# Kernel tuning notes

Measured on AMD Instinct MI355X. Metric: run time of the kernel, lower is better.

Reference implementation:

```python
import jax, jax.numpy as jnp
import numpy as np

N_HEAD = 8
D = 512
D_K = D // N_HEAD  # 64
B, S = 8, 1024


def setup_inputs() -> dict:
    key = jax.random.key(0)
    ks = jax.random.split(key, 7)
    scale = 1.0 / np.sqrt(D)  # ~ torch Linear init range
    return {
        "q": jax.random.normal(ks[0], (B, S, D), dtype=jnp.float32),
        "k": jax.random.normal(ks[1], (B, S, D), dtype=jnp.float32),
        "v": jax.random.normal(ks[2], (B, S, D), dtype=jnp.float32),
        # per-head Q/K projection weights, torch Linear convention W:[out,in]=[d_k,d]
        "Wq": jax.random.uniform(ks[3], (N_HEAD, D_K, D), jnp.float32, -scale, scale),
        "Wk": jax.random.uniform(ks[4], (N_HEAD, D_K, D), jnp.float32, -scale, scale),
        "Wv": jax.random.uniform(ks[5], (D_K, D), jnp.float32, -scale, scale),
        "Wo": jax.random.uniform(ks[6], (D, D_K), jnpp := jnp.float32, -1.0 / np.sqrt(D_K), 1.0 / np.sqrt(D_K)),
    }


def reference(q, k, v, Wq, Wk, Wv, Wo):
    # shared V projection: [B,S,d_k]
    vs = jnp.einsum("bsd,ed->bse", v, Wv)
    # batched per-head Q/K projections: [B,H,S,d_k]
    qh = jnp.einsum("bsd,hed->bhse", q, Wq)
    kh = jnp.einsum("bsd,hed->bhse", k, Wk)
    inv_sqrt_dk = 1.0 / jnp.sqrt(jnp.asarray(D_K, q.dtype))
    # scores [B,H,Sq,Sk], softmax over keys
    scores = jnp.einsum("bhqe,bhke->bhqk", qh * inv_sqrt_dk, kh)
    attn = jax.nn.softmax(scores, axis=-1)
    # shared V across heads, then mean over heads (interpretable combine)
    heads = jnp.einsum("bhqk,bke->bhqe", attn, vs)  # [B,H,S,d_k]
    head = heads.mean(axis=1)                        # [B,S,d_k]
    out = jnp.einsum("bse,de->bsd", head, Wo)        # [B,S,d]
    # torch.stack(attention) stacks over heads first -> [H,B,Sq,Sk]
    attn_stacked = jnp.transpose(attn, (1, 0, 2, 3))
    return out, attn_stacked
```

## Files before the change

### kernel.cpp

```cpp
#include <hip/hip_runtime.h>


using short8 = __attribute__((ext_vector_type(8))) short;
using f32x4  = __attribute__((ext_vector_type(4))) float;

static __device__ __forceinline__ short f2bf(float f) {
    union { float f; unsigned u; } x; x.f = f;
    unsigned r = x.u + 0x7fffu + ((x.u >> 16) & 1u);
    return (short)(r >> 16);
}
static __device__ __forceinline__ float bfhi2f(unsigned hi_bits) {
    union { unsigned u; float f; } x; x.u = hi_bits;
    return x.f;
}

__global__ __launch_bounds__(256) void proj_all(
    const float* __restrict__ q, const float* __restrict__ k,
    const float* __restrict__ v,
    const float* __restrict__ Wq, const float* __restrict__ Wk,
    const float* __restrict__ Wv,
    short* __restrict__ qh, short* __restrict__ kh, short* __restrict__ vt)
{
    __shared__ short As[128][40];
    __shared__ short Bs[128][40];

    const int y = blockIdx.y;
    const float* A; const float* W; short* out; int N; float scale; int mode; int n0;
    if (y < 4)      { A = q; W = Wq; out = qh; N = 512; scale = 0.125f; mode = 0; n0 = y << 7; }
    else if (y < 8) { A = k; W = Wk; out = kh; N = 512; scale = 1.0f;   mode = 0; n0 = (y - 4) << 7; }
    else            { A = v; W = Wv; out = vt; N = 64;  scale = 1.0f;   mode = 2; n0 = 0; }

    const int K = 512;
    const int tid  = threadIdx.x;
    const int m0   = blockIdx.x * 128;
    const int lane = tid & 63, wave = tid >> 6;
    const int wm   = (wave & 1) * 64, wn = (wave >> 1) * 64;
    const int lrow = lane & 15, lq = lane >> 4;

    f32x4 acc[4][4] = {};

    for (int k0 = 0; k0 < K; k0 += 32) {
#pragma unroll
        for (int i = 0; i < 4; ++i) {
            int c = tid + i * 256;
            int row = c >> 3, c4 = c & 7;
            float4 vv = *(const float4*)(A + (size_t)(m0 + row) * K + k0 + c4 * 4);
            short* dst = &As[row][c4 * 4];
            dst[0] = f2bf(vv.x); dst[1] = f2bf(vv.y); dst[2] = f2bf(vv.z); dst[3] = f2bf(vv.w);
        }
#pragma unroll
        for (int i = 0; i < 4; ++i) {
            int c = tid + i * 256;
            int row = c >> 3, c4 = c & 7;
            int gn = n0 + row;
            float4 vv = make_float4(0.f, 0.f, 0.f, 0.f);
            if (gn < N) vv = *(const float4*)(W + (size_t)gn * K + k0 + c4 * 4);
            short* dst = &Bs[row][c4 * 4];
            dst[0] = f2bf(vv.x); dst[1] = f2bf(vv.y); dst[2] = f2bf(vv.z); dst[3] = f2bf(vv.w);
        }
        __syncthreads();

        short8 af[4], bw[4];
#pragma unroll
        for (int i = 0; i < 4; ++i)
            af[i] = *(const short8*)&As[wm + i * 16 + lrow][lq * 8];
#pragma unroll
        for (int j = 0; j < 4; ++j)
            bw[j] = *(const short8*)&Bs[wn + j * 16 + lrow][lq * 8];
#pragma unroll
        for (int i = 0; i < 4; ++i)
#pragma unroll
            for (int j = 0; j < 4; ++j)
                acc[i][j] = __builtin_amdgcn_mfma_f32_16x16x32_bf16(af[i], bw[j], acc[i][j], 0, 0, 0);
        __syncthreads();
    }

#pragma unroll
    for (int i = 0; i < 4; ++i) {
#pragma unroll
        for (int j = 0; j < 4; ++j) {
#pragma unroll
            for (int r = 0; r < 4; ++r) {
                int m = m0 + wm + i * 16 + lq * 4 + r;
                int n = n0 + wn + j * 16 + lrow;
                if (n >= N) continue;
                float val = acc[i][j][r] * scale;
                if (mode == 0) {
                    int b = m >> 10, s = m & 1023;
                    int hh = n >> 6, e = n & 63;
                    out[(((size_t)(b * 8 + hh) * 1024 + s) << 6) + e] = f2bf(val);
                } else {
                    int b = m >> 10, s = m & 1023;
                    out[(((size_t)b * 64 + n) << 10) + s] = f2bf(val);
                }
            }
        }
    }
}

__global__ __launch_bounds__(256) void gemm_out(
    const float* __restrict__ A, const float* __restrict__ W,
    float* __restrict__ out, int M, int N, int K)
{
    __shared__ short As[128][40];
    __shared__ short Bs[128][40];

    const int tid  = threadIdx.x;
    const int m0   = blockIdx.x * 128;
    const int n0   = blockIdx.y * 128;
    const int lane = tid & 63, wave = tid >> 6;
    const int wm   = (wave & 1) * 64, wn = (wave >> 1) * 64;
    const int lrow = lane & 15, lq = lane >> 4;

    f32x4 acc[4][4] = {};

    for (int k0 = 0; k0 < K; k0 += 32) {
#pragma unroll
        for (int i = 0; i < 4; ++i) {
            int c = tid + i * 256;
            int row = c >> 3, c4 = c & 7;
            float4 vv = *(const float4*)(A + (size_t)(m0 + row) * K + k0 + c4 * 4);
            short* dst = &As[row][c4 * 4];
            dst[0] = f2bf(vv.x); dst[1] = f2bf(vv.y); dst[2] = f2bf(vv.z); dst[3] = f2bf(vv.w);
        }
#pragma unroll
        for (int i = 0; i < 4; ++i) {
            int c = tid + i * 256;
            int row = c >> 3, c4 = c & 7;
            int gn = n0 + row;
            float4 vv = make_float4(0.f, 0.f, 0.f, 0.f);
            if (gn < N) vv = *(const float4*)(W + (size_t)gn * K + k0 + c4 * 4);
            short* dst = &Bs[row][c4 * 4];
            dst[0] = f2bf(vv.x); dst[1] = f2bf(vv.y); dst[2] = f2bf(vv.z); dst[3] = f2bf(vv.w);
        }
        __syncthreads();

        short8 af[4], bw[4];
#pragma unroll
        for (int i = 0; i < 4; ++i)
            af[i] = *(const short8*)&As[wm + i * 16 + lrow][lq * 8];
#pragma unroll
        for (int j = 0; j < 4; ++j)
            bw[j] = *(const short8*)&Bs[wn + j * 16 + lrow][lq * 8];
#pragma unroll
        for (int i = 0; i < 4; ++i)
#pragma unroll
            for (int j = 0; j < 4; ++j)
                acc[i][j] = __builtin_amdgcn_mfma_f32_16x16x32_bf16(af[i], bw[j], acc[i][j], 0, 0, 0);
        __syncthreads();
    }

#pragma unroll
    for (int i = 0; i < 4; ++i)
#pragma unroll
        for (int j = 0; j < 4; ++j)
#pragma unroll
            for (int r = 0; r < 4; ++r) {
                int m = m0 + wm + i * 16 + lq * 4 + r;
                int n = n0 + wn + j * 16 + lrow;
                if (n >= N) continue;
                out[(size_t)m * N + n] = acc[i][j][r];
            }
}

__global__ __launch_bounds__(512) void attn_fused(
    const short* __restrict__ qh,
    const short* __restrict__ kh,
    const short* __restrict__ vt,
    float* __restrict__ attn_out,
    float* __restrict__ head)
{
    __shared__ short qs[128][72];
    __shared__ short ks[128][72];
    __shared__ short vts[64][136];
    __shared__ short pa[8][16][136];

    const int bh = blockIdx.x;
    const int b = bh >> 3, h = bh & 7;
    const int qbase = blockIdx.y << 7;
    const int tid  = threadIdx.x;
    const int lane = tid & 63, wave = tid >> 6;
    const int lrow = lane & 15, lq = lane >> 4;

    const short* qp = qh + ((size_t)bh << 16);
    const short* kp = kh + ((size_t)bh << 16);
    const short* vp = vt + ((size_t)b << 16);

#pragma unroll
    for (int i = 0; i < 2; ++i) {
        int c = tid + i * 512;
        int row = c >> 3, c8 = c & 7;
        *(uint4*)&qs[row][c8 * 8] = *(const uint4*)(qp + (size_t)(qbase + row) * 64 + c8 * 8);
    }
    __syncthreads();

    short8 qf[2];
#pragma unroll
    for (int kk = 0; kk < 2; ++kk)
        qf[kk] = *(const short8*)&qs[wave * 16 + lrow][kk * 32 + lq * 8];

    float sume[4] = {0.f, 0.f, 0.f, 0.f};
    for (int kt = 0; kt < 1024; kt += 128) {
        __syncthreads();
#pragma unroll
        for (int i = 0; i < 2; ++i) {
            int c = tid + i * 512;
            int row = c >> 3, c8 = c & 7;
            *(uint4*)&ks[row][c8 * 8] = *(const uint4*)(kp + (size_t)(kt + row) * 64 + c8 * 8);
        }
        __syncthreads();
#pragma unroll
        for (int j = 0; j < 8; ++j) {
            f32x4 sc = {0.f, 0.f, 0.f, 0.f};
            short8 kb0 = *(const short8*)&ks[j * 16 + lrow][lq * 8];
            short8 kb1 = *(const short8*)&ks[j * 16 + lrow][32 + lq * 8];
            sc = __builtin_amdgcn_mfma_f32_16x16x32_bf16(qf[0], kb0, sc, 0, 0, 0);
            sc = __builtin_amdgcn_mfma_f32_16x16x32_bf16(qf[1], kb1, sc, 0, 0, 0);
#pragma unroll
            for (int r = 0; r < 4; ++r) sume[r] += __expf(sc[r]);
        }
    }
#pragma unroll
    for (int m = 1; m <= 8; m <<= 1)
#pragma unroll
        for (int r = 0; r < 4; ++r) sume[r] += __shfl_xor(sume[r], m, 64);
    float rinv[4];
#pragma unroll
    for (int r = 0; r < 4; ++r) rinv[r] = 1.0f / sume[r];

    f32x4 hacc[4] = {};
    for (int kt = 0; kt < 1024; kt += 128) {
        __syncthreads();
#pragma unroll
        for (int i = 0; i < 2; ++i) {
            int c = tid + i * 512;
            int row = c >> 3, c8 = c & 7;
            *(uint4*)&ks[row][c8 * 8] = *(const uint4*)(kp + (size_t)(kt + row) * 64 + c8 * 8);
        }
#pragma unroll
        for (int i = 0; i < 2; ++i) {
            int c = tid + i * 512;
            int row = c >> 4, c8 = c & 15;
            *(uint4*)&vts[row][c8 * 8] = *(const uint4*)(vp + ((size_t)row << 10) + kt + c8 * 8);
        }
        __syncthreads();

#pragma unroll
        for (int j = 0; j < 8; ++j) {
            f32x4 sc = {0.f, 0.f, 0.f, 0.f};
            short8 kb0 = *(const short8*)&ks[j * 16 + lrow][lq * 8];
            short8 kb1 = *(const short8*)&ks[j * 16 + lrow][32 + lq * 8];
            sc = __builtin_amdgcn_mfma_f32_16x16x32_bf16(qf[0], kb0, sc, 0, 0, 0);
            sc = __builtin_amdgcn_mfma_f32_16x16x32_bf16(qf[1], kb1, sc, 0, 0, 0);
#pragma unroll
            for (int r = 0; r < 4; ++r)
                pa[wave][lq * 4 + r][j * 16 + lrow] = f2bf(__expf(sc[r]) * rinv[r]);
        }

        size_t abase = (((size_t)(h * 8 + b) * 1024 + qbase + wave * 16) << 10) + kt;
#pragma unroll
        for (int i = 0; i < 4; ++i) {
            int c = lane + i * 64;
            int row = c >> 4, c8 = c & 15;
            uint4 pk = *(const uint4*)&pa[wave][row][c8 * 8];
            f32x4 v0, v1;
            v0.x = bfhi2f(pk.x << 16); v0.y = bfhi2f(pk.x & 0xffff0000u);
            v0.z = bfhi2f(pk.y << 16); v0.w = bfhi2f(pk.y & 0xffff0000u);
            v1.x = bfhi2f(pk.z << 16); v1.y = bfhi2f(pk.z & 0xffff0000u);
            v1.z = bfhi2f(pk.w << 16); v1.w = bfhi2f(pk.w & 0xffff0000u);
            float* gdst = attn_out + abase + ((size_t)row << 10) + c8 * 8;
            __builtin_nontemporal_store(v0, (f32x4*)gdst);
            __builtin_nontemporal_store(v1, (f32x4*)(gdst + 4));
        }

#pragma unroll
        for (int kk = 0; kk < 4; ++kk) {
            short8 af = *(const short8*)&pa[wave][lrow][kk * 32 + lq * 8];
#pragma unroll
            for (int cc = 0; cc < 4; ++cc) {
                short8 bv = *(const short8*)&vts[cc * 16 + lrow][kk * 32 + lq * 8];
                hacc[cc] = __builtin_amdgcn_mfma_f32_16x16x32_bf16(af, bv, hacc[cc], 0, 0, 0);
            }
        }
    }

#pragma unroll
    for (int cc = 0; cc < 4; ++cc)
#pragma unroll
        for (int r = 0; r < 4; ++r) {
            float v = hacc[cc][r] * 0.125f;
            atomicAdd(&head[(((size_t)b * 1024 + qbase + wave * 16 + lq * 4 + r) << 6) + cc * 16 + lrow], v);
        }
}

extern "C" void kernel_launch(void* const* d_in, const int* in_sizes, int n_in,
                              void* d_out, int out_size, void* d_ws, size_t ws_size,
                              hipStream_t stream)
{
    (void)in_sizes; (void)n_in; (void)out_size; (void)ws_size;

    const float* q  = (const float*)d_in[0];
    const float* k  = (const float*)d_in[1];
    const float* v  = (const float*)d_in[2];
    const float* Wq = (const float*)d_in[3];
    const float* Wk = (const float*)d_in[4];
    const float* Wv = (const float*)d_in[5];
    const float* Wo = (const float*)d_in[6];

    float* out  = (float*)d_out;
    float* attn = out + (size_t)8 * 1024 * 512;

    char* ws = (char*)d_ws;
    short* qh  = (short*)(ws);
    short* kh  = (short*)(ws + ((size_t)8  << 20));
    short* vt  = (short*)(ws + ((size_t)16 << 20));
    float* head = (float*)(ws + ((size_t)17 << 20));

    (void)hipMemsetAsync(head, 0, (size_t)8 * 1024 * 64 * sizeof(float), stream);

    proj_all<<<dim3(64, 9), 256, 0, stream>>>(q, k, v, Wq, Wk, Wv, qh, kh, vt);

    attn_fused<<<dim3(64, 8), 512, 0, stream>>>(qh, kh, vt, attn, head);

    gemm_out<<<dim3(64, 4), 256, 0, stream>>>(head, Wo, out, 8192, 512, 64);
}
```

Measured before the change: 455.1 us.

## Alias Q and P tiles in LDS, reverse second K pass, widen GEMM K-step

The attention kernel overlays the Q staging buffer and the per-wave probability tile in one shared-memory union and declares a min-blocks launch bound, both meant to let more workgroups fit per CU. The second pass now walks key tiles in reverse, so the last K tile from the first pass is reused without reloading it. The projection GEMM uses a 64-wide K step, halving barrier count. The output GEMM is specialized for K=64 with a single load phase. This trades register/LDS headroom for occupancy and may cause spills under the tighter launch bound.

Result: slower. 526.8 us (+15.7%).

```diff
diff --git a/kernel.cpp b/kernel.cpp
--- a/kernel.cpp
+++ b/kernel.cpp
@@ -21,8 +21,8 @@
     const float* __restrict__ Wv,
     short* __restrict__ qh, short* __restrict__ kh, short* __restrict__ vt)
 {
-    __shared__ short As[128][40];
-    __shared__ short Bs[128][40];
+    __shared__ short As[128][72];
+    __shared__ short Bs[128][72];
 
     const int y = blockIdx.y;
     const float* A; const float* W; short* out; int N; float scale; int mode; int n0;
@@ -39,39 +39,42 @@
 
     f32x4 acc[4][4] = {};
 
-    for (int k0 = 0; k0 < K; k0 += 32) {
-#pragma unroll
-        for (int i = 0; i < 4; ++i) {
+    for (int k0 = 0; k0 < K; k0 += 64) {
+#pragma unroll
+        for (int i = 0; i < 8; ++i) {
             int c = tid + i * 256;
-            int row = c >> 3, c4 = c & 7;
-            float4 vv = *(const float4*)(A + (size_t)(m0 + row) * K + k0 + c4 * 4);
-            short* dst = &As[row][c4 * 4];
+            int row = c >> 4, c16 = c & 15;
+            float4 vv = *(const float4*)(A + (size_t)(m0 + row) * K + k0 + c16 * 4);
+            short* dst = &As[row][c16 * 4];
             dst[0] = f2bf(vv.x); dst[1] = f2bf(vv.y); dst[2] = f2bf(vv.z); dst[3] = f2bf(vv.w);
         }
 #pragma unroll
-        for (int i = 0; i < 4; ++i) {
+        for (int i = 0; i < 8; ++i) {
             int c = tid + i * 256;
-            int row = c >> 3, c4 = c & 7;
+            int row = c >> 4, c16 = c & 15;
             int gn = n0 + row;
             float4 vv = make_float4(0.f, 0.f, 0.f, 0.f);
-            if (gn < N) vv = *(const float4*)(W + (size_t)gn * K + k0 + c4 * 4);
-            short* dst = &Bs[row][c4 * 4];
+            if (gn < N) vv = *(const float4*)(W + (size_t)gn * K + k0 + c16 * 4);
+            short* dst = &Bs[row][c16 * 4];
             dst[0] = f2bf(vv.x); dst[1] = f2bf(vv.y); dst[2] = f2bf(vv.z); dst[3] = f2bf(vv.w);
         }
         __syncthreads();
 
-        short8 af[4], bw[4];
-#pragma unroll
-        for (int i = 0; i < 4; ++i)
-            af[i] = *(const short8*)&As[wm + i * 16 + lrow][lq * 8];
-#pragma unroll
-        for (int j = 0; j < 4; ++j)
-            bw[j] = *(const short8*)&Bs[wn + j * 16 + lrow][lq * 8];
-#pragma unroll
-        for (int i = 0; i < 4; ++i)
+#pragma unroll
+        for (int kk = 0; kk < 2; ++kk) {
+            short8 af[4], bw[4];
+#pragma unroll
+            for (int i = 0; i < 4; ++i)
+                af[i] = *(const short8*)&As[wm + i * 16 + lrow][kk * 32 + lq * 8];
 #pragma unroll
             for (int j = 0; j < 4; ++j)
-                acc[i][j] = __builtin_amdgcn_mfma_f32_16x16x32_bf16(af[i], bw[j], acc[i][j], 0, 0, 0);
+                bw[j] = *(const short8*)&Bs[wn + j * 16 + lrow][kk * 32 + lq * 8];
+#pragma unroll
+            for (int i = 0; i < 4; ++i)
+#pragma unroll
+                for (int j = 0; j < 4; ++j)
+                    acc[i][j] = __builtin_amdgcn_mfma_f32_16x16x32_bf16(af[i], bw[j], acc[i][j], 0, 0, 0);
+        }
         __syncthreads();
     }
 
@@ -100,10 +103,10 @@
 
 __global__ __launch_bounds__(256) void gemm_out(
     const float* __restrict__ A, const float* __restrict__ W,
-    float* __restrict__ out, int M, int N, int K)
+    float* __restrict__ out)
 {
-    __shared__ short As[128][40];
-    __shared__ short Bs[128][40];
+    __shared__ short As[128][72];
+    __shared__ short Bs[128][72];
 
     const int tid  = threadIdx.x;
     const int m0   = blockIdx.x * 128;
@@ -114,40 +117,38 @@
 
     f32x4 acc[4][4] = {};
 
-    for (int k0 = 0; k0 < K; k0 += 32) {
-#pragma unroll
-        for (int i = 0; i < 4; ++i) {
-            int c = tid + i * 256;
-            int row = c >> 3, c4 = c & 7;
-            float4 vv = *(const float4*)(A + (size_t)(m0 + row) * K + k0 + c4 * 4);
-            short* dst = &As[row][c4 * 4];
-            dst[0] = f2bf(vv.x); dst[1] = f2bf(vv.y); dst[2] = f2bf(vv.z); dst[3] = f2bf(vv.w);
-        }
-#pragma unroll
-        for (int i = 0; i < 4; ++i) {
-            int c = tid + i * 256;
-            int row = c >> 3, c4 = c & 7;
-            int gn = n0 + row;
-            float4 vv = make_float4(0.f, 0.f, 0.f, 0.f);
-            if (gn < N) vv = *(const float4*)(W + (size_t)gn * K + k0 + c4 * 4);
-            short* dst = &Bs[row][c4 * 4];
-            dst[0] = f2bf(vv.x); dst[1] = f2bf(vv.y); dst[2] = f2bf(vv.z); dst[3] = f2bf(vv.w);
-        }
-        __syncthreads();
-
+#pragma unroll
+    for (int i = 0; i < 8; ++i) {
+        int c = tid + i * 256;
+        int row = c >> 4, c16 = c & 15;
+        float4 vv = *(const float4*)(A + (size_t)(m0 + row) * 64 + c16 * 4);
+        short* dst = &As[row][c16 * 4];
+        dst[0] = f2bf(vv.x); dst[1] = f2bf(vv.y); dst[2] = f2bf(vv.z); dst[3] = f2bf(vv.w);
+    }
+#pragma unroll
+    for (int i = 0; i < 8; ++i) {
+        int c = tid + i * 256;
+        int row = c >> 4, c16 = c & 15;
+        float4 vv = *(const float4*)(W + (size_t)(n0 + row) * 64 + c16 * 4);
+        short* dst = &Bs[row][c16 * 4];
+        dst[0] = f2bf(vv.x); dst[1] = f2bf(vv.y); dst[2] = f2bf(vv.z); dst[3] = f2bf(vv.w);
+    }
+    __syncthreads();
+
+#pragma unroll
+    for (int kk = 0; kk < 2; ++kk) {
         short8 af[4], bw[4];
 #pragma unroll
         for (int i = 0; i < 4; ++i)
-            af[i] = *(const short8*)&As[wm + i * 16 + lrow][lq * 8];
+            af[i] = *(const short8*)&As[wm + i * 16 + lrow][kk * 32 + lq * 8];
 #pragma unroll
         for (int j = 0; j < 4; ++j)
-            bw[j] = *(const short8*)&Bs[wn + j * 16 + lrow][lq * 8];
+            bw[j] = *(const short8*)&Bs[wn + j * 16 + lrow][kk * 32 + lq * 8];
 #pragma unroll
         for (int i = 0; i < 4; ++i)
 #pragma unroll
             for (int j = 0; j < 4; ++j)
                 acc[i][j] = __builtin_amdgcn_mfma_f32_16x16x32_bf16(af[i], bw[j], acc[i][j], 0, 0, 0);
-        __syncthreads();
     }
 
 #pragma unroll
@@ -158,22 +159,25 @@
             for (int r = 0; r < 4; ++r) {
                 int m = m0 + wm + i * 16 + lq * 4 + r;
                 int n = n0 + wn + j * 16 + lrow;
-                if (n >= N) continue;
-                out[(size_t)m * N + n] = acc[i][j][r];
+                out[(size_t)m * 512 + n] = acc[i][j][r];
             }
 }
 
-__global__ __launch_bounds__(512) void attn_fused(
+union SharedQP {
+    short qs[128][72];
+    short pa[8][16][136];
+};
+
+__global__ __launch_bounds__(512, 4) void attn_fused(
     const short* __restrict__ qh,
     const short* __restrict__ kh,
     const short* __restrict__ vt,
     float* __restrict__ attn_out,
     float* __restrict__ head)
 {
-    __shared__ short qs[128][72];
+    __shared__ SharedQP u;
     __shared__ short ks[128][72];
     __shared__ short vts[64][136];
-    __shared__ short pa[8][16][136];
 
     const int bh = blockIdx.x;
     const int b = bh >> 3, h = bh & 7;
@@ -190,14 +194,14 @@
     for (int i = 0; i < 2; ++i) {
         int c = tid + i * 512;
         int row = c >> 3, c8 = c & 7;
-        *(uint4*)&qs[row][c8 * 8] = *(const uint4*)(qp + (size_t)(qbase + row) * 64 + c8 * 8);
+        *(uint4*)&u.qs[row][c8 * 8] = *(const uint4*)(qp + (size_t)(qbase + row) * 64 + c8 * 8);
     }
     __syncthreads();
 
     short8 qf[2];
 #pragma unroll
     for (int kk = 0; kk < 2; ++kk)
-        qf[kk] = *(const short8*)&qs[wave * 16 + lrow][kk * 32 + lq * 8];
+        qf[kk] = *(const short8*)&u.qs[wave * 16 + lrow][kk * 32 + lq * 8];
 
     float sume[4] = {0.f, 0.f, 0.f, 0.f};
     for (int kt = 0; kt < 1024; kt += 128) {
@@ -229,13 +233,16 @@
     for (int r = 0; r < 4; ++r) rinv[r] = 1.0f / sume[r];
 
     f32x4 hacc[4] = {};
-    for (int kt = 0; kt < 1024; kt += 128) {
-        __syncthreads();
-#pragma unroll
-        for (int i = 0; i < 2; ++i) {
-            int c = tid + i * 512;
-            int row = c >> 3, c8 = c & 7;
-            *(uint4*)&ks[row][c8 * 8] = *(const uint4*)(kp + (size_t)(kt + row) * 64 + c8 * 8);
+    for (int it = 0; it < 8; ++it) {
+        const int kt = 896 - (it << 7);
+        __syncthreads();
+        if (it != 0) {
+#pragma unroll
+            for (int i = 0; i < 2; ++i) {
+                int c = tid + i * 512;
+                int row = c >> 3, c8 = c & 7;
+                *(uint4*)&ks[row][c8 * 8] = *(const uint4*)(kp + (size_t)(kt + row) * 64 + c8 * 8);
+            }
         }
 #pragma unroll
         for (int i = 0; i < 2; ++i) {
@@ -254,7 +261,7 @@
             sc = __builtin_amdgcn_mfma_f32_16x16x32_bf16(qf[1], kb1, sc, 0, 0, 0);
 #pragma unroll
             for (int r = 0; r < 4; ++r)
-                pa[wave][lq * 4 + r][j * 16 + lrow] = f2bf(__expf(sc[r]) * rinv[r]);
+                u.pa[wave][lq * 4 + r][j * 16 + lrow] = f2bf(__expf(sc[r]) * rinv[r]);
         }
 
         size_t abase = (((size_t)(h * 8 + b) * 1024 + qbase + wave * 16) << 10) + kt;
@@ -262,7 +269,7 @@
         for (int i = 0; i < 4; ++i) {
             int c = lane + i * 64;
             int row = c >> 4, c8 = c & 15;
-            uint4 pk = *(const uint4*)&pa[wave][row][c8 * 8];
+            uint4 pk = *(const uint4*)&u.pa[wave][row][c8 * 8];
             f32x4 v0, v1;
             v0.x = bfhi2f(pk.x << 16); v0.y = bfhi2f(pk.x & 0xffff0000u);
             v0.z = bfhi2f(pk.y << 16); v0.w = bfhi2f(pk.y & 0xffff0000u);
@@ -275,7 +282,7 @@
 
 #pragma unroll
         for (int kk = 0; kk < 4; ++kk) {
-            short8 af = *(const short8*)&pa[wave][lrow][kk * 32 + lq * 8];
+            short8 af = *(const short8*)&u.pa[wave][lrow][kk * 32 + lq * 8];
 #pragma unroll
             for (int cc = 0; cc < 4; ++cc) {
                 short8 bv = *(const short8*)&vts[cc * 16 + lrow][kk * 32 + lq * 8];
@@ -322,5 +329,5 @@
 
     attn_fused<<<dim3(64, 8), 512, 0, stream>>>(qh, kh, vt, attn, head);
 
-    gemm_out<<<dim3(64, 4), 256, 0, stream>>>(head, Wo, out, 8192, 512, 64);
-}
+    gemm_out<<<dim3(64, 4), 256, 0, stream>>>(head, Wo, out);
+}
```

## Register-prefetch K/V tiles in attention and specialize output GEMM for K=64

Applied to the files above, without the earlier changes.

The attention kernel now loads the next K (and V^T) tile into registers while the current tile is being computed, then stores it to LDS at the top of the next iteration. The goal is to hide global-load latency behind the MFMA and exp work. The output GEMM is specialized to the fixed K=64, so the whole tile is loaded once with a single barrier, and the probability scratch row stride is padded to reduce LDS bank conflicts. In exchange, register pressure rises in a 512-thread kernel, and the GEMM loses generality, with no bounds checks.

After: 428.8 us. 5.8% less time.

```diff
diff --git a/kernel.cpp b/kernel.cpp
--- a/kernel.cpp
+++ b/kernel.cpp
@@ -100,10 +100,10 @@
 
 __global__ __launch_bounds__(256) void gemm_out(
     const float* __restrict__ A, const float* __restrict__ W,
-    float* __restrict__ out, int M, int N, int K)
+    float* __restrict__ out)
 {
-    __shared__ short As[128][40];
-    __shared__ short Bs[128][40];
+    __shared__ short As[128][72];
+    __shared__ short Bs[128][72];
 
     const int tid  = threadIdx.x;
     const int m0   = blockIdx.x * 128;
@@ -114,40 +114,38 @@
 
     f32x4 acc[4][4] = {};
 
-    for (int k0 = 0; k0 < K; k0 += 32) {
-#pragma unroll
-        for (int i = 0; i < 4; ++i) {
-            int c = tid + i * 256;
-            int row = c >> 3, c4 = c & 7;
-            float4 vv = *(const float4*)(A + (size_t)(m0 + row) * K + k0 + c4 * 4);
-            short* dst = &As[row][c4 * 4];
-            dst[0] = f2bf(vv.x); dst[1] = f2bf(vv.y); dst[2] = f2bf(vv.z); dst[3] = f2bf(vv.w);
-        }
-#pragma unroll
-        for (int i = 0; i < 4; ++i) {
-            int c = tid + i * 256;
-            int row = c >> 3, c4 = c & 7;
-            int gn = n0 + row;
-            float4 vv = make_float4(0.f, 0.f, 0.f, 0.f);
-            if (gn < N) vv = *(const float4*)(W + (size_t)gn * K + k0 + c4 * 4);
-            short* dst = &Bs[row][c4 * 4];
-            dst[0] = f2bf(vv.x); dst[1] = f2bf(vv.y); dst[2] = f2bf(vv.z); dst[3] = f2bf(vv.w);
-        }
-        __syncthreads();
-
+#pragma unroll
+    for (int i = 0; i < 8; ++i) {
+        int c = tid + i * 256;
+        int row = c >> 4, c16 = c & 15;
+        float4 vv = *(const float4*)(A + (size_t)(m0 + row) * 64 + c16 * 4);
+        short* dst = &As[row][c16 * 4];
+        dst[0] = f2bf(vv.x); dst[1] = f2bf(vv.y); dst[2] = f2bf(vv.z); dst[3] = f2bf(vv.w);
+    }
+#pragma unroll
+    for (int i = 0; i < 8; ++i) {
+        int c = tid + i * 256;
+        int row = c >> 4, c16 = c & 15;
+        float4 vv = *(const float4*)(W + (size_t)(n0 + row) * 64 + c16 * 4);
+        short* dst = &Bs[row][c16 * 4];
+        dst[0] = f2bf(vv.x); dst[1] = f2bf(vv.y); dst[2] = f2bf(vv.z); dst[3] = f2bf(vv.w);
+    }
+    __syncthreads();
+
+#pragma unroll
+    for (int kk = 0; kk < 2; ++kk) {
         short8 af[4], bw[4];
 #pragma unroll
         for (int i = 0; i < 4; ++i)
-            af[i] = *(const short8*)&As[wm + i * 16 + lrow][lq * 8];
+            af[i] = *(const short8*)&As[wm + i * 16 + lrow][kk * 32 + lq * 8];
 #pragma unroll
         for (int j = 0; j < 4; ++j)
-            bw[j] = *(const short8*)&Bs[wn + j * 16 + lrow][lq * 8];
+            bw[j] = *(const short8*)&Bs[wn + j * 16 + lrow][kk * 32 + lq * 8];
 #pragma unroll
         for (int i = 0; i < 4; ++i)
 #pragma unroll
             for (int j = 0; j < 4; ++j)
                 acc[i][j] = __builtin_amdgcn_mfma_f32_16x16x32_bf16(af[i], bw[j], acc[i][j], 0, 0, 0);
-        __syncthreads();
     }
 
 #pragma unroll
@@ -158,8 +156,7 @@
             for (int r = 0; r < 4; ++r) {
                 int m = m0 + wm + i * 16 + lq * 4 + r;
                 int n = n0 + wn + j * 16 + lrow;
-                if (n >= N) continue;
-                out[(size_t)m * N + n] = acc[i][j][r];
+                out[(size_t)m * 512 + n] = acc[i][j][r];
             }
 }
 
@@ -173,7 +170,7 @@
     __shared__ short qs[128][72];
     __shared__ short ks[128][72];
     __shared__ short vts[64][136];
-    __shared__ short pa[8][16][136];
+    __shared__ short pa[8][16][152];
 
     const int bh = blockIdx.x;
     const int b = bh >> 3, h = bh & 7;
@@ -199,16 +196,28 @@
     for (int kk = 0; kk < 2; ++kk)
         qf[kk] = *(const short8*)&qs[wave * 16 + lrow][kk * 32 + lq * 8];
 
+    uint4 kreg[2];
+#pragma unroll
+    for (int i = 0; i < 2; ++i) {
+        int c = tid + i * 512;
+        kreg[i] = *(const uint4*)(kp + (size_t)(c >> 3) * 64 + (c & 7) * 8);
+    }
     float sume[4] = {0.f, 0.f, 0.f, 0.f};
     for (int kt = 0; kt < 1024; kt += 128) {
         __syncthreads();
 #pragma unroll
         for (int i = 0; i < 2; ++i) {
             int c = tid + i * 512;
-            int row = c >> 3, c8 = c & 7;
-            *(uint4*)&ks[row][c8 * 8] = *(const uint4*)(kp + (size_t)(kt + row) * 64 + c8 * 8);
-        }
-        __syncthreads();
+            *(uint4*)&ks[c >> 3][(c & 7) * 8] = kreg[i];
+        }
+        __syncthreads();
+        if (kt + 128 < 1024) {
+#pragma unroll
+            for (int i = 0; i < 2; ++i) {
+                int c = tid + i * 512;
+                kreg[i] = *(const uint4*)(kp + (size_t)(kt + 128 + (c >> 3)) * 64 + (c & 7) * 8);
+            }
+        }
 #pragma unroll
         for (int j = 0; j < 8; ++j) {
             f32x4 sc = {0.f, 0.f, 0.f, 0.f};
@@ -220,6 +229,15 @@
             for (int r = 0; r < 4; ++r) sume[r] += __expf(sc[r]);
         }
     }
+
+    uint4 vreg[2];
+#pragma unroll
+    for (int i = 0; i < 2; ++i) {
+        int c = tid + i * 512;
+        kreg[i] = *(const uint4*)(kp + (size_t)(c >> 3) * 64 + (c & 7) * 8);
+        vreg[i] = *(const uint4*)(vp + ((size_t)(c >> 4) << 10) + (c & 15) * 8);
+    }
+
 #pragma unroll
     for (int m = 1; m <= 8; m <<= 1)
 #pragma unroll
@@ -234,16 +252,18 @@
 #pragma unroll
         for (int i = 0; i < 2; ++i) {
             int c = tid + i * 512;
-            int row = c >> 3, c8 = c & 7;
-            *(uint4*)&ks[row][c8 * 8] = *(const uint4*)(kp + (size_t)(kt + row) * 64 + c8 * 8);
-        }
-#pragma unroll
-        for (int i = 0; i < 2; ++i) {
-            int c = tid + i * 512;
-            int row = c >> 4, c8 = c & 15;
-            *(uint4*)&vts[row][c8 * 8] = *(const uint4*)(vp + ((size_t)row << 10) + kt + c8 * 8);
-        }
-        __syncthreads();
+            *(uint4*)&ks[c >> 3][(c & 7) * 8] = kreg[i];
+            *(uint4*)&vts[c >> 4][(c & 15) * 8] = vreg[i];
+        }
+        __syncthreads();
+        if (kt + 128 < 1024) {
+#pragma unroll
+            for (int i = 0; i < 2; ++i) {
+                int c = tid + i * 512;
+                kreg[i] = *(const uint4*)(kp + (size_t)(kt + 128 + (c >> 3)) * 64 + (c & 7) * 8);
+                vreg[i] = *(const uint4*)(vp + ((size_t)(c >> 4) << 10) + kt + 128 + (c & 15) * 8);
+            }
+        }
 
 #pragma unroll
         for (int j = 0; j < 8; ++j) {
@@ -322,5 +342,5 @@
 
     attn_fused<<<dim3(64, 8), 512, 0, stream>>>(qh, kh, vt, attn, head);
 
-    gemm_out<<<dim3(64, 4), 256, 0, stream>>>(head, Wo, out, 8192, 512, 64);
-}
+    gemm_out<<<dim3(64, 4), 256, 0, stream>>>(head, Wo, out);
+}
```
